# Kernel optimization log

Measured on AMD Instinct MI355X. Metric: run time of the kernel, lower is better.

## Reference

```python
import jax, jax.numpy as jnp
import numpy as np

Q_BITS = 8
GELU_A = -0.2888
GELU_B = -1.769
INV_SQRT2 = 0.7071067811865476


def _ste_round(x):
    # straight-through round (identity grad)
    return x + jax.lax.stop_gradient(jnp.round(x) - x)


def fake_quant_weight(w):
    # per-tensor symmetric int8 fake quant
    qmax = 2.0 ** (Q_BITS - 1) - 1.0  # 127
    s = jnp.maximum(jnp.max(jnp.abs(w)), 1e-8) / qmax
    q = jnp.clip(_ste_round(w / s), -qmax - 1.0, qmax)
    return q * s


def fake_quant_act(x):
    # per-tensor asymmetric uint8 fake quant
    levels = 2.0 ** Q_BITS - 1.0  # 255
    xmin = jax.lax.stop_gradient(jnp.min(x))
    xmax = jax.lax.stop_gradient(jnp.max(x))
    s = jnp.maximum(xmax - xmin, 1e-8) / levels
    zp = jnp.round(-xmin / s)
    q = jnp.clip(_ste_round(x / s) + zp, 0.0, levels)
    return (q - zp) * s


def int_gelu(x):
    # I-BERT polynomial GELU: gelu(x) = x * 0.5 * (1 + L(x/sqrt(2)))
    # L(t) = sign(t) * (a * (clip(|t|, 0, -b) + b)^2 + 1)
    t = x * INV_SQRT2
    at = jnp.minimum(jnp.abs(t), -GELU_B)
    L = jnp.sign(t) * (GELU_A * (at + GELU_B) ** 2 + 1.0)
    return x * 0.5 * (1.0 + L)


def setup_inputs() -> dict:
    key = jax.random.key(0)
    k = jax.random.split(key, 5)
    B, S, D, H = 64, 197, 768, 3072
    x = jax.random.normal(k[0], (B, S, D), dtype=jnp.float32)
    w1 = jax.random.normal(k[1], (H, D), dtype=jnp.float32) * (1.0 / np.sqrt(D))
    b1 = jax.random.normal(k[2], (H,), dtype=jnp.float32) * 0.02
    w2 = jax.random.normal(k[3], (D, H), dtype=jnp.float32) * (1.0 / np.sqrt(H))
    b2 = jax.random.normal(k[4], (D,), dtype=jnp.float32) * 0.02
    return {"x": x, "w1": w1, "b1": b1, "w2": w2, "b2": b2}


def reference(x, w1, b1, w2, b2):
    # QuantLinear 1: fake-quant act + weight, then GEMM
    xq = fake_quant_act(x)
    h = jnp.einsum('bsd,hd->bsh', xq, fake_quant_weight(w1)) + b1
    # IntGELU (dropout is identity in eval)
    g = int_gelu(h)
    # QuantLinear 2
    gq = fake_quant_act(g)
    out = jnp.einsum('bsh,dh->bsd', gq, fake_quant_weight(w2)) + b2
    return out
```

## Files before the change

kernel.cpp:

```cpp
#include <hip/hip_runtime.h>
#include <stdint.h>
#include <stddef.h>

typedef int v4i  __attribute__((ext_vector_type(4)));
typedef int v16i __attribute__((ext_vector_type(16)));
typedef _Float16 vh8 __attribute__((ext_vector_type(8)));

#define GELU_A   (-0.2888f)
#define GELU_B   (-1.769f)
#define INV_SQRT2 0.70710678118654752440f

#define GLD16(gp, lp) __builtin_amdgcn_global_load_lds( \
    (const __attribute__((address_space(1))) unsigned int*)(gp), \
    (__attribute__((address_space(3))) unsigned int*)(lp), 16, 0, 0)

#define WAIT_VM6 0x0F76
#define WAIT_VM0 0x0F70


__device__ __forceinline__ unsigned enc_f(float f){
  unsigned u = __float_as_uint(f);
  return (u & 0x80000000u) ? ~u : (u | 0x80000000u);
}
__device__ __forceinline__ float dec_f(unsigned e){
  unsigned u = (e & 0x80000000u) ? (e & 0x7FFFFFFFu) : ~e;
  return __uint_as_float(u);
}

__device__ __forceinline__ float int_gelu_f(float x){
  float t = x * INV_SQRT2;
  float at = fminf(fabsf(t), 1.769f);
  float u = at + GELU_B;
  float p = GELU_A * (u * u) + 1.0f;
  float L = (t > 0.0f) ? p : ((t < 0.0f) ? -p : 0.0f);
  return x * 0.5f * (1.0f + L);
}

__global__ __launch_bounds__(256) void reduce_stats(
    const float4* __restrict__ x, int nx4,
    const float4* __restrict__ w1, int n14,
    const float4* __restrict__ w2, int n24,
    unsigned* __restrict__ sc)
{
  __shared__ float ra[256], rb[256];
  const int tid = threadIdx.x;
  const int b = blockIdx.x;
  if (b < 1024){
    float lmin = 3.4e38f, lmax = -3.4e38f;
    for (long i = (long)b * 256 + tid; i < nx4; i += 1024L * 256L){
      float4 v = x[i];
      lmin = fminf(lmin, fminf(fminf(v.x, v.y), fminf(v.z, v.w)));
      lmax = fmaxf(lmax, fmaxf(fmaxf(v.x, v.y), fmaxf(v.z, v.w)));
    }
    ra[tid] = lmin; rb[tid] = lmax;
    __syncthreads();
    for (int s = 128; s > 0; s >>= 1){
      if (tid < s){ ra[tid] = fminf(ra[tid], ra[tid + s]); rb[tid] = fmaxf(rb[tid], rb[tid + s]); }
      __syncthreads();
    }
    if (tid == 0){
      atomicMin(&sc[0], enc_f(ra[0]));
      atomicMax(&sc[2], enc_f(rb[0]));
    }
  } else {
    const float4* w; int n4; int slot; int bl;
    if (b < 1152){ w = w1; n4 = n14; slot = 3; bl = b - 1024; }
    else         { w = w2; n4 = n24; slot = 4; bl = b - 1152; }
    float la = 0.0f;
    for (long i = (long)bl * 256 + tid; i < n4; i += 128L * 256L){
      float4 v = w[i];
      la = fmaxf(la, fmaxf(fmaxf(fabsf(v.x), fabsf(v.y)), fmaxf(fabsf(v.z), fabsf(v.w))));
    }
    ra[tid] = la;
    __syncthreads();
    for (int s = 128; s > 0; s >>= 1){
      if (tid < s) ra[tid] = fmaxf(ra[tid], ra[tid + s]);
      __syncthreads();
    }
    if (tid == 0) atomicMax(&sc[slot], __float_as_uint(ra[0]));
  }
}

__global__ __launch_bounds__(256) void quant_all(
    const float4* __restrict__ x, unsigned* __restrict__ qx, long nx4,
    const float* __restrict__ w1, const float* __restrict__ w2,
    int8_t* __restrict__ qw1, int8_t* __restrict__ qw2,
    int* __restrict__ rs1, int* __restrict__ rs2,
    const unsigned* __restrict__ sc, int H, int D)
{
  const int tid = threadIdx.x;
  const int b = blockIdx.x;
  if (b < 2048){
    const float vmin = dec_f(sc[0]);
    const float vmax = dec_f(sc[2]);
    const float s  = fmaxf(vmax - vmin, 1e-8f) / 255.0f;
    const float zp = rintf(-vmin / s);
    for (long i = (long)b * 256 + tid; i < nx4; i += 2048L * 256L){
      float4 v = x[i];
      int q0 = (int)fminf(fmaxf(rintf(v.x / s) + zp, 0.0f), 255.0f) - 128;
      int q1 = (int)fminf(fmaxf(rintf(v.y / s) + zp, 0.0f), 255.0f) - 128;
      int q2 = (int)fminf(fmaxf(rintf(v.z / s) + zp, 0.0f), 255.0f) - 128;
      int q3 = (int)fminf(fmaxf(rintf(v.w / s) + zp, 0.0f), 255.0f) - 128;
      qx[i] = ((unsigned)(q0 & 255)) | ((unsigned)(q1 & 255) << 8) |
              ((unsigned)(q2 & 255) << 16) | ((unsigned)(q3 & 255) << 24);
    }
  } else {
    __shared__ int red[256];
    const int wb = b - 2048;
    const float* w; int8_t* q; int* rs; int K; int n; float s;
    if (wb < H){ w = w1; q = qw1; rs = rs1; K = D; n = wb;
                 s = fmaxf(__uint_as_float(sc[3]), 1e-8f) / 127.0f; }
    else       { w = w2; q = qw2; rs = rs2; K = H; n = wb - H;
                 s = fmaxf(__uint_as_float(sc[4]), 1e-8f) / 127.0f; }
    int sum = 0;
    for (int k = tid; k < K; k += 256){
      float v = w[(size_t)n * K + k];
      float qf = fminf(fmaxf(rintf(v / s), -128.0f), 127.0f);
      int qi = (int)qf;
      q[(size_t)n * K + k] = (int8_t)qi;
      sum += qi;
    }
    red[tid] = sum;
    __syncthreads();
    for (int st = 128; st > 0; st >>= 1){
      if (tid < st) red[tid] += red[tid + st];
      __syncthreads();
    }
    if (tid == 0) rs[n] = red[0];
  }
}

__global__ __launch_bounds__(256) void quant_g(
    const vh8* __restrict__ g, uint2* __restrict__ qg, long n8,
    const unsigned* __restrict__ sc)
{
  const float gmin = dec_f(sc[1]), gmax = dec_f(sc[5]);
  const float qs  = fmaxf(gmax - gmin, 1e-8f) / 255.0f;
  const float qzp = rintf(-gmin / qs);
  const long stride = (long)gridDim.x * blockDim.x;
  for (long i = (long)blockIdx.x * blockDim.x + threadIdx.x; i < n8; i += stride){
    vh8 v = g[i];
    unsigned lo = 0, hi = 0;
#pragma unroll
    for (int j = 0; j < 4; j++){
      int q = (int)fminf(fmaxf(rintf((float)v[j] / qs) + qzp, 0.0f), 255.0f) - 128;
      lo |= ((unsigned)(q & 255)) << (8 * j);
    }
#pragma unroll
    for (int j = 0; j < 4; j++){
      int q = (int)fminf(fmaxf(rintf((float)v[4 + j] / qs) + qzp, 0.0f), 255.0f) - 128;
      hi |= ((unsigned)(q & 255)) << (8 * j);
    }
    uint2 o; o.x = lo; o.y = hi;
    qg[i] = o;
  }
}

template<int MODE>
__global__ __launch_bounds__(256, 2) void gemm_i8(
    const int8_t* __restrict__ A, const int8_t* __restrict__ Bm,
    const int* __restrict__ rowsum, const float* __restrict__ bias,
    void* __restrict__ Cout, int M, int N, int K,
    unsigned* __restrict__ sc)
{
  __shared__ __align__(16) int8_t lds[3][24576];

  const int tid  = threadIdx.x;
  const int lane = tid & 63;
  const int wave = tid >> 6;
  const int l31  = lane & 31;
  const int kh   = lane >> 5;
  const int n0   = blockIdx.x * 256;
  const int m0   = blockIdx.y * 128;
  const int wm   = (wave >> 1) * 64;
  const int wn   = (wave & 1) * 128;

  int aoffs[2], boffs[4];
  const int ldstA[2] = { wave * 2048, wave * 2048 + 1024 };
  const int ldstB[4] = { 8192 + wave * 4096,        8192 + wave * 4096 + 1024,
                         8192 + wave * 4096 + 2048, 8192 + wave * 4096 + 3072 };
#pragma unroll
  for (int t = 0; t < 2; t++){
    int rowl = wave * 32 + t * 16 + (lane >> 2);
    int csw  = ((lane & 3) ^ ((rowl >> 1) & 3)) << 4;
    int ga = m0 + rowl; if (ga >= M) ga = M - 1;
    aoffs[t] = ga * K + csw;
  }
#pragma unroll
  for (int t = 0; t < 4; t++){
    int rowl = wave * 64 + t * 16 + (lane >> 2);
    int csw  = ((lane & 3) ^ ((rowl >> 1) & 3)) << 4;
    boffs[t] = (n0 + rowl) * K + csw;
  }

  const int w2  = (l31 >> 1) & 3;
  const int sA0 = (kh ^ w2) << 4;
  int arow[2], brow[4];
#pragma unroll
  for (int mi = 0; mi < 2; mi++) arow[mi] = (wm + mi * 32 + l31) * 64;
#pragma unroll
  for (int nj = 0; nj < 4; nj++) brow[nj] = (wn + nj * 32 + l31) * 64;

  v16i acc[2][4] = {};
  const int NT = K >> 6;

#pragma unroll
  for (int t = 0; t < 2; t++) GLD16(A  + aoffs[t],      &lds[0][ldstA[t]]);
#pragma unroll
  for (int t = 0; t < 4; t++) GLD16(Bm + boffs[t],      &lds[0][ldstB[t]]);
#pragma unroll
  for (int t = 0; t < 2; t++) GLD16(A  + aoffs[t] + 64, &lds[1][ldstA[t]]);
#pragma unroll
  for (int t = 0; t < 4; t++) GLD16(Bm + boffs[t] + 64, &lds[1][ldstB[t]]);

  for (int kt = 0; kt < NT; kt++){
    const int8_t* buf = lds[kt % 3];
    if (kt + 1 < NT) __builtin_amdgcn_s_waitcnt(WAIT_VM6);
    else             __builtin_amdgcn_s_waitcnt(WAIT_VM0);
    __builtin_amdgcn_s_barrier();
    __builtin_amdgcn_sched_barrier(0);

    v4i af[2][2], bf[2][4];
#pragma unroll
    for (int kk = 0; kk < 2; kk++){
      const int sb = sA0 ^ (kk << 5);
#pragma unroll
      for (int mi = 0; mi < 2; mi++)
        af[kk][mi] = *(const v4i*)(buf + arow[mi] + sb);
#pragma unroll
      for (int nj = 0; nj < 4; nj++)
        bf[kk][nj] = *(const v4i*)(buf + 8192 + brow[nj] + sb);
    }

    if (kt + 2 < NT){
      int8_t* nbuf = lds[(kt + 2) % 3];
      const int ko = (kt + 2) << 6;
#pragma unroll
      for (int t = 0; t < 2; t++) GLD16(A  + aoffs[t] + ko, nbuf + ldstA[t]);
#pragma unroll
      for (int t = 0; t < 4; t++) GLD16(Bm + boffs[t] + ko, nbuf + ldstB[t]);
    }

#pragma unroll
    for (int kk = 0; kk < 2; kk++)
#pragma unroll
      for (int mi = 0; mi < 2; mi++)
#pragma unroll
        for (int nj = 0; nj < 4; nj++)
          acc[mi][nj] = __builtin_amdgcn_mfma_i32_32x32x32_i8(af[kk][mi], bf[kk][nj], acc[mi][nj], 0, 0, 0);
  }

  float s_h, off_h;
  if constexpr (MODE == 1){
    float gmin = dec_f(sc[1]), gmax = dec_f(sc[5]);
    float sg = fmaxf(gmax - gmin, 1e-8f) / 255.0f;
    float zp = rintf(-gmin / sg);
    float sw = fmaxf(__uint_as_float(sc[4]), 1e-8f) / 127.0f;
    s_h = sg * sw; off_h = 128.0f - zp;
  } else {
    float xmin = dec_f(sc[0]), xmax = dec_f(sc[2]);
    float sx = fmaxf(xmax - xmin, 1e-8f) / 255.0f;
    float zp = rintf(-xmin / sx);
    float sw = fmaxf(__uint_as_float(sc[3]), 1e-8f) / 127.0f;
    s_h = sx * sw; off_h = 128.0f - zp;
  }
  float qs = 1.0f, qzp = 0.0f;
  if constexpr (MODE == 2){
    float gmin = dec_f(sc[1]), gmax = dec_f(sc[5]);
    qs = fmaxf(gmax - gmin, 1e-8f) / 255.0f;
    qzp = rintf(-gmin / qs);
  }

  float lmin = 3.4e38f, lmax = -3.4e38f;
#pragma unroll
  for (int nj = 0; nj < 4; nj++){
    const int n = n0 + wn + nj * 32 + l31;
    const float rsv = off_h * (float)rowsum[n];
    const float bv = bias[n];
#pragma unroll
    for (int mi = 0; mi < 2; mi++){
      const int mbase = m0 + wm + mi * 32 + 4 * kh;
#pragma unroll
      for (int r = 0; r < 16; r++){
        const int m = mbase + (r & 3) + 8 * (r >> 2);
        if (m < M){
          float h = s_h * ((float)acc[mi][nj][r] + rsv) + bv;
          if constexpr (MODE == 0){
            float gv = int_gelu_f(h);
            lmin = fminf(lmin, gv); lmax = fmaxf(lmax, gv);
          } else if constexpr (MODE == 3){
            float gv = int_gelu_f(h);
            lmin = fminf(lmin, gv); lmax = fmaxf(lmax, gv);
            ((_Float16*)Cout)[(size_t)m * N + n] = (_Float16)gv;
          } else if constexpr (MODE == 2){
            float gv = int_gelu_f(h);
            float qf = fminf(fmaxf(rintf(gv / qs) + qzp, 0.0f), 255.0f);
            ((int8_t*)Cout)[(size_t)m * N + n] = (int8_t)((int)qf - 128);
          } else {
            ((float*)Cout)[(size_t)m * N + n] = h;
          }
        }
      }
    }
  }

  if constexpr (MODE == 0 || MODE == 3){
    __syncthreads();
    float* redA = (float*)&lds[0][0];
    float* redB = ((float*)&lds[0][0]) + 256;
    redA[tid] = lmin; redB[tid] = lmax;
    __syncthreads();
    for (int st = 128; st > 0; st >>= 1){
      if (tid < st){
        redA[tid] = fminf(redA[tid], redA[tid + st]);
        redB[tid] = fmaxf(redB[tid], redB[tid + st]);
      }
      __syncthreads();
    }
    if (tid == 0){
      atomicMin(&sc[1], enc_f(redA[0]));
      atomicMax(&sc[5], enc_f(redB[0]));
    }
  }
}

extern "C" void kernel_launch(void* const* d_in, const int* in_sizes, int n_in,
                              void* d_out, int out_size, void* d_ws, size_t ws_size,
                              hipStream_t stream)
{
  const float* x  = (const float*)d_in[0];
  const float* w1 = (const float*)d_in[1];
  const float* b1 = (const float*)d_in[2];
  const float* w2 = (const float*)d_in[3];
  const float* b2 = (const float*)d_in[4];
  float* out = (float*)d_out;

  const int H = in_sizes[2];
  const int D = in_sizes[4];
  const int M = in_sizes[0] / D;

  char* ws = (char*)d_ws;
  unsigned* sc = (unsigned*)ws;
  size_t off = 256;
  int8_t* qx  = (int8_t*)(ws + off); off += (size_t)M * D;
  int8_t* qw1 = (int8_t*)(ws + off); off += (size_t)H * D;
  int8_t* qw2 = (int8_t*)(ws + off); off += (size_t)D * H;
  int* rs1 = (int*)(ws + off); off += (size_t)H * 4;
  int* rs2 = (int*)(ws + off); off += 4096;
  int8_t* qg  = (int8_t*)(ws + off); off += (size_t)M * H;
  _Float16* g16 = (_Float16*)(ws + off);
  const size_t need_big = off + (size_t)M * H * 2;
  (void)n_in; (void)out_size;

  hipMemsetAsync(sc, 0xFF, 8, stream);
  hipMemsetAsync(sc + 2, 0x00, 16, stream);

  reduce_stats<<<dim3(1280), dim3(256), 0, stream>>>(
      (const float4*)x, M * D / 4,
      (const float4*)w1, H * D / 4,
      (const float4*)w2, D * H / 4, sc);

  quant_all<<<dim3(2048 + H + D), dim3(256), 0, stream>>>(
      (const float4*)x, (unsigned*)qx, (long)M * D / 4,
      w1, w2, qw1, qw2, rs1, rs2, sc, H, D);

  const dim3 g1(H / 256, (M + 127) / 128), g2(D / 256, (M + 127) / 128), blk(256);

  if (ws_size >= need_big){
    gemm_i8<3><<<g1, blk, 0, stream>>>(qx, qw1, rs1, b1, g16, M, H, D, sc);
    quant_g<<<dim3(2048), blk, 0, stream>>>(
        (const vh8*)g16, (uint2*)qg, (long)M * H / 8, sc);
  } else {
    gemm_i8<0><<<g1, blk, 0, stream>>>(qx, qw1, rs1, b1, nullptr, M, H, D, sc);
    gemm_i8<2><<<g1, blk, 0, stream>>>(qx, qw1, rs1, b1, qg, M, H, D, sc);
  }

  gemm_i8<1><<<g2, blk, 0, stream>>>(qg, qw2, rs2, b2, out, M, D, H, sc);
}
```

Before: 331.8 us.

## Enlarge GEMM tiles to 512-thread blocks with split-K-half ping-pong pipeline

Templates the int8 GEMM on block and warp tile sizes and moves it to 512-thread blocks with 256-row M tiles (256x256 for GEMM1, 256x128 for GEMM2). The main loop now splits each 64-wide K step into two halves, interleaving the A and B prefetch issue with LDS fragment loads and adding barriers around MFMA bursts raised with s_setprio. The aim is more operand reuse per tile and better overlap of global-to-LDS loads with matrix math. In exchange it adds more barriers per iteration, uses more LDS per block, and means fewer blocks for the small N=768 GEMM.

```diff
diff --git a/kernel.cpp b/kernel.cpp
--- a/kernel.cpp
+++ b/kernel.cpp
@@ -14,8 +14,10 @@
     (const __attribute__((address_space(1))) unsigned int*)(gp), \
     (__attribute__((address_space(3))) unsigned int*)(lp), 16, 0, 0)
 
-#define WAIT_VM6 0x0F76
-#define WAIT_VM0 0x0F70
+#define WAIT_VM4   0x0F74
+#define WAIT_VM3   0x0F73
+#define WAIT_VM0   0x0F70
+#define WAIT_LGKM0 0xC07F
 
 
 __device__ __forceinline__ unsigned enc_f(float f){
@@ -156,29 +158,34 @@
   }
 }
 
-template<int MODE>
-__global__ __launch_bounds__(256, 2) void gemm_i8(
+template<int MODE, int BM, int BN, int WM, int WN>
+__global__ __launch_bounds__(512) void gemm_i8(
     const int8_t* __restrict__ A, const int8_t* __restrict__ Bm,
     const int* __restrict__ rowsum, const float* __restrict__ bias,
     void* __restrict__ Cout, int M, int N, int K,
     unsigned* __restrict__ sc)
 {
-  __shared__ __align__(16) int8_t lds[3][24576];
+  constexpr int NWN  = BN / WN;
+  constexpr int MI   = WM / 32;
+  constexpr int NJ   = WN / 32;
+  constexpr int NBG  = BN / 128;
+  constexpr int LDSB = 16384 + BN * 64;
+  constexpr int WAIT_STEADY = (NBG == 2) ? WAIT_VM4 : WAIT_VM3;
+  __shared__ __align__(16) int8_t lds[3][LDSB];
 
   const int tid  = threadIdx.x;
   const int lane = tid & 63;
   const int wave = tid >> 6;
   const int l31  = lane & 31;
   const int kh   = lane >> 5;
-  const int n0   = blockIdx.x * 256;
-  const int m0   = blockIdx.y * 128;
-  const int wm   = (wave >> 1) * 64;
-  const int wn   = (wave & 1) * 128;
-
-  int aoffs[2], boffs[4];
+  const int n0   = blockIdx.x * BN;
+  const int m0   = blockIdx.y * BM;
+  const int wm   = (wave / NWN) * WM;
+  const int wn   = (wave % NWN) * WN;
+
+  int aoffs[2], boffs[NBG];
   const int ldstA[2] = { wave * 2048, wave * 2048 + 1024 };
-  const int ldstB[4] = { 8192 + wave * 4096,        8192 + wave * 4096 + 1024,
-                         8192 + wave * 4096 + 2048, 8192 + wave * 4096 + 3072 };
+  int ldstB[NBG];
 #pragma unroll
   for (int t = 0; t < 2; t++){
     int rowl = wave * 32 + t * 16 + (lane >> 2);
@@ -187,67 +194,91 @@
     aoffs[t] = ga * K + csw;
   }
 #pragma unroll
-  for (int t = 0; t < 4; t++){
-    int rowl = wave * 64 + t * 16 + (lane >> 2);
+  for (int t = 0; t < NBG; t++){
+    int rowl = wave * 16 * NBG + t * 16 + (lane >> 2);
     int csw  = ((lane & 3) ^ ((rowl >> 1) & 3)) << 4;
     boffs[t] = (n0 + rowl) * K + csw;
+    ldstB[t] = 16384 + wave * NBG * 1024 + t * 1024;
   }
 
   const int w2  = (l31 >> 1) & 3;
   const int sA0 = (kh ^ w2) << 4;
-  int arow[2], brow[4];
-#pragma unroll
-  for (int mi = 0; mi < 2; mi++) arow[mi] = (wm + mi * 32 + l31) * 64;
-#pragma unroll
-  for (int nj = 0; nj < 4; nj++) brow[nj] = (wn + nj * 32 + l31) * 64;
-
-  v16i acc[2][4] = {};
+  int arow[MI], brow[NJ];
+#pragma unroll
+  for (int mi = 0; mi < MI; mi++) arow[mi] = (wm + mi * 32 + l31) * 64;
+#pragma unroll
+  for (int nj = 0; nj < NJ; nj++) brow[nj] = 16384 + (wn + nj * 32 + l31) * 64;
+
+  v16i acc[MI][NJ] = {};
   const int NT = K >> 6;
 
 #pragma unroll
-  for (int t = 0; t < 2; t++) GLD16(A  + aoffs[t],      &lds[0][ldstA[t]]);
-#pragma unroll
-  for (int t = 0; t < 4; t++) GLD16(Bm + boffs[t],      &lds[0][ldstB[t]]);
-#pragma unroll
-  for (int t = 0; t < 2; t++) GLD16(A  + aoffs[t] + 64, &lds[1][ldstA[t]]);
-#pragma unroll
-  for (int t = 0; t < 4; t++) GLD16(Bm + boffs[t] + 64, &lds[1][ldstB[t]]);
-
+  for (int bt = 0; bt < 2; bt++){
+#pragma unroll
+    for (int t = 0; t < 2;   t++) GLD16(A  + aoffs[t] + bt * 64, &lds[bt][ldstA[t]]);
+#pragma unroll
+    for (int t = 0; t < NBG; t++) GLD16(Bm + boffs[t] + bt * 64, &lds[bt][ldstB[t]]);
+  }
+  __builtin_amdgcn_s_waitcnt(WAIT_STEADY);
+  __builtin_amdgcn_s_barrier();
+
+  int bcur = 0, bst = 2;
   for (int kt = 0; kt < NT; kt++){
-    const int8_t* buf = lds[kt % 3];
-    if (kt + 1 < NT) __builtin_amdgcn_s_waitcnt(WAIT_VM6);
-    else             __builtin_amdgcn_s_waitcnt(WAIT_VM0);
+    const int8_t* buf = &lds[bcur][0];
+    int8_t* nbuf = &lds[bst][0];
+    const bool pf = (kt + 2 < NT);
+    const int ko = (kt + 2) << 6;
+
+    v4i af[MI], bf[NJ];
+
+#pragma unroll
+    for (int mi = 0; mi < MI; mi++) af[mi] = *(const v4i*)(buf + arow[mi] + sA0);
+#pragma unroll
+    for (int nj = 0; nj < NJ; nj++) bf[nj] = *(const v4i*)(buf + brow[nj] + sA0);
+    if (pf){
+#pragma unroll
+      for (int t = 0; t < 2; t++) GLD16(A + aoffs[t] + ko, nbuf + ldstA[t]);
+    }
+    __builtin_amdgcn_sched_barrier(0);
     __builtin_amdgcn_s_barrier();
-    __builtin_amdgcn_sched_barrier(0);
-
-    v4i af[2][2], bf[2][4];
-#pragma unroll
-    for (int kk = 0; kk < 2; kk++){
-      const int sb = sA0 ^ (kk << 5);
-#pragma unroll
-      for (int mi = 0; mi < 2; mi++)
-        af[kk][mi] = *(const v4i*)(buf + arow[mi] + sb);
-#pragma unroll
-      for (int nj = 0; nj < 4; nj++)
-        bf[kk][nj] = *(const v4i*)(buf + 8192 + brow[nj] + sb);
-    }
-
-    if (kt + 2 < NT){
-      int8_t* nbuf = lds[(kt + 2) % 3];
-      const int ko = (kt + 2) << 6;
-#pragma unroll
-      for (int t = 0; t < 2; t++) GLD16(A  + aoffs[t] + ko, nbuf + ldstA[t]);
-#pragma unroll
-      for (int t = 0; t < 4; t++) GLD16(Bm + boffs[t] + ko, nbuf + ldstB[t]);
-    }
-
-#pragma unroll
-    for (int kk = 0; kk < 2; kk++)
-#pragma unroll
-      for (int mi = 0; mi < 2; mi++)
-#pragma unroll
-        for (int nj = 0; nj < 4; nj++)
-          acc[mi][nj] = __builtin_amdgcn_mfma_i32_32x32x32_i8(af[kk][mi], bf[kk][nj], acc[mi][nj], 0, 0, 0);
+    __builtin_amdgcn_s_waitcnt(WAIT_LGKM0);
+    __builtin_amdgcn_sched_barrier(0);
+    __builtin_amdgcn_s_setprio(1);
+#pragma unroll
+    for (int mi = 0; mi < MI; mi++)
+#pragma unroll
+      for (int nj = 0; nj < NJ; nj++)
+        acc[mi][nj] = __builtin_amdgcn_mfma_i32_32x32x32_i8(af[mi], bf[nj], acc[mi][nj], 0, 0, 0);
+    __builtin_amdgcn_s_setprio(0);
+    __builtin_amdgcn_sched_barrier(0);
+    __builtin_amdgcn_s_barrier();
+
+#pragma unroll
+    for (int mi = 0; mi < MI; mi++) af[mi] = *(const v4i*)(buf + arow[mi] + (sA0 ^ 32));
+#pragma unroll
+    for (int nj = 0; nj < NJ; nj++) bf[nj] = *(const v4i*)(buf + brow[nj] + (sA0 ^ 32));
+    if (pf){
+#pragma unroll
+      for (int t = 0; t < NBG; t++) GLD16(Bm + boffs[t] + ko, nbuf + ldstB[t]);
+    }
+    __builtin_amdgcn_sched_barrier(0);
+    if (pf) __builtin_amdgcn_s_waitcnt(WAIT_STEADY);
+    else    __builtin_amdgcn_s_waitcnt(WAIT_VM0);
+    __builtin_amdgcn_s_barrier();
+    __builtin_amdgcn_s_waitcnt(WAIT_LGKM0);
+    __builtin_amdgcn_sched_barrier(0);
+    __builtin_amdgcn_s_setprio(1);
+#pragma unroll
+    for (int mi = 0; mi < MI; mi++)
+#pragma unroll
+      for (int nj = 0; nj < NJ; nj++)
+        acc[mi][nj] = __builtin_amdgcn_mfma_i32_32x32x32_i8(af[mi], bf[nj], acc[mi][nj], 0, 0, 0);
+    __builtin_amdgcn_s_setprio(0);
+    __builtin_amdgcn_sched_barrier(0);
+    __builtin_amdgcn_s_barrier();
+
+    bcur = (bcur == 2) ? 0 : bcur + 1;
+    bst  = (bst  == 2) ? 0 : bst  + 1;
   }
 
   float s_h, off_h;
@@ -273,12 +304,12 @@
 
   float lmin = 3.4e38f, lmax = -3.4e38f;
 #pragma unroll
-  for (int nj = 0; nj < 4; nj++){
+  for (int nj = 0; nj < NJ; nj++){
     const int n = n0 + wn + nj * 32 + l31;
     const float rsv = off_h * (float)rowsum[n];
     const float bv = bias[n];
 #pragma unroll
-    for (int mi = 0; mi < 2; mi++){
+    for (int mi = 0; mi < MI; mi++){
       const int mbase = m0 + wm + mi * 32 + 4 * kh;
 #pragma unroll
       for (int r = 0; r < 16; r++){
@@ -307,10 +338,10 @@
   if constexpr (MODE == 0 || MODE == 3){
     __syncthreads();
     float* redA = (float*)&lds[0][0];
-    float* redB = ((float*)&lds[0][0]) + 256;
+    float* redB = ((float*)&lds[0][0]) + 512;
     redA[tid] = lmin; redB[tid] = lmax;
     __syncthreads();
-    for (int st = 128; st > 0; st >>= 1){
+    for (int st = 256; st > 0; st >>= 1){
       if (tid < st){
         redA[tid] = fminf(redA[tid], redA[tid + st]);
         redB[tid] = fmaxf(redB[tid], redB[tid + st]);
@@ -364,16 +395,16 @@
       (const float4*)x, (unsigned*)qx, (long)M * D / 4,
       w1, w2, qw1, qw2, rs1, rs2, sc, H, D);
 
-  const dim3 g1(H / 256, (M + 127) / 128), g2(D / 256, (M + 127) / 128), blk(256);
+  const dim3 g1(H / 256, (M + 255) / 256), g2(D / 128, (M + 255) / 256), blk(512);
 
   if (ws_size >= need_big){
-    gemm_i8<3><<<g1, blk, 0, stream>>>(qx, qw1, rs1, b1, g16, M, H, D, sc);
-    quant_g<<<dim3(2048), blk, 0, stream>>>(
+    gemm_i8<3, 256, 256, 128, 64><<<g1, blk, 0, stream>>>(qx, qw1, rs1, b1, g16, M, H, D, sc);
+    quant_g<<<dim3(2048), dim3(256), 0, stream>>>(
         (const vh8*)g16, (uint2*)qg, (long)M * H / 8, sc);
   } else {
-    gemm_i8<0><<<g1, blk, 0, stream>>>(qx, qw1, rs1, b1, nullptr, M, H, D, sc);
-    gemm_i8<2><<<g1, blk, 0, stream>>>(qx, qw1, rs1, b1, qg, M, H, D, sc);
-  }
-
-  gemm_i8<1><<<g2, blk, 0, stream>>>(qg, qw2, rs2, b2, out, M, D, H, sc);
-}
+    gemm_i8<0, 256, 256, 128, 64><<<g1, blk, 0, stream>>>(qx, qw1, rs1, b1, nullptr, M, H, D, sc);
+    gemm_i8<2, 256, 256, 128, 64><<<g1, blk, 0, stream>>>(qx, qw1, rs1, b1, qg, M, H, D, sc);
+  }
+
+  gemm_i8<1, 256, 128, 64, 64><<<g2, blk, 0, stream>>>(qg, qw2, rs2, b2, out, M, D, H, sc);
+}
```

Result: no change. 329.8 us (-0.6%).
